# Optimization experiments

Hardware: AMD Instinct MI355X
Metric: run time of the kernel (lower is better)

The kernel has to match this reference:

```python
import jax, jax.numpy as jnp
import numpy as np


def _gcn(x, src, dst, W, b, n):
    # symmetric normalization: deg computed on edges WITH self-loops (weights 1)
    deg = jax.ops.segment_sum(jnp.ones_like(src, dtype=x.dtype), dst, num_segments=n)
    dinv = jnp.where(deg > 0, jax.lax.rsqrt(deg), 0.0)
    norm = dinv[src] * dinv[dst]              # [E+n]
    xw = x @ W                                # [n, out] transform first (cheaper)
    msg = xw[src] * norm[:, None]             # gather + edge scale
    return jax.ops.segment_sum(msg, dst, num_segments=n) + b


def setup_inputs() -> dict:
    key = jax.random.key(0)
    ks = jax.random.split(key, 8)
    N, E = 100_000, 1_280_000
    x = jax.random.normal(ks[0], (N, 18), dtype=jnp.float32)
    edge_index = jax.random.randint(ks[1], (2, E), 0, N, dtype=jnp.int32)
    W1 = jax.random.normal(ks[2], (18, 32), dtype=jnp.float32) * 0.2
    b1 = jnp.zeros((32,), dtype=jnp.float32)
    W2 = jax.random.normal(ks[3], (32, 64), dtype=jnp.float32) * 0.15
    b2 = jnp.zeros((64,), dtype=jnp.float32)
    Wfc = jax.random.normal(ks[4], (64, 2), dtype=jnp.float32) * 0.1
    bfc = jnp.zeros((2,), dtype=jnp.float32)
    return {"x": x, "edge_index": edge_index, "W1": W1, "b1": b1,
            "W2": W2, "b2": b2, "Wfc": Wfc, "bfc": bfc}


def reference(x, edge_index, W1, b1, W2, b2, Wfc, bfc):
    n = x.shape[0]
    loop = jnp.arange(n, dtype=edge_index.dtype)
    src = jnp.concatenate([edge_index[0], loop])   # add self-loops (PyG default)
    dst = jnp.concatenate([edge_index[1], loop])
    h = jax.nn.relu(_gcn(x, src, dst, W1, b1, n))
    h = jax.nn.relu(_gcn(h, src, dst, W2, b2, n))
    logits = h @ Wfc + bfc
    return jax.nn.log_softmax(logits, axis=1)
```

## Files before the change

### kernel.cpp

```cpp
#include <hip/hip_runtime.h>
#include <hip/hip_fp16.h>
#include <math.h>


#define TPB 256
#define BSH 8
#define BNODES 256
#define MAXBUCK 512
#define CH 8192
#define CAPSH 13
#define CAP (1 << CAPSH)

__global__ void k_part(const int* __restrict__ src, const int* __restrict__ dst,
                       int* __restrict__ bcursor, int* __restrict__ eb,
                       __half* __restrict__ u1h, __half* __restrict__ u2h,
                       int E, int n, int nbuck) {
    __shared__ int lh[MAXBUCK];
    __shared__ int lbase[MAXBUCK];
    int t = threadIdx.x;
    if (blockIdx.x == 0 && t < 32) {
        u1h[(size_t)n * 32 + t] = __float2half_rn(0.f);
        u2h[(size_t)n * 32 + t] = __float2half_rn(0.f);
    }
    int chunk0 = blockIdx.x * CH;
    int end = min(chunk0 + CH, E);
    const int4* dst4 = (const int4*)dst;
    const int4* src4 = (const int4*)src;
    for (int i = t; i < nbuck; i += TPB) lh[i] = 0;
    __syncthreads();
    for (int e4 = chunk0 / 4 + t; e4 * 4 < end; e4 += TPB) {
        int base = e4 * 4;
        int4 d = dst4[e4];
        if (base + 0 < end) atomicAdd(&lh[d.x >> BSH], 1);
        if (base + 1 < end) atomicAdd(&lh[d.y >> BSH], 1);
        if (base + 2 < end) atomicAdd(&lh[d.z >> BSH], 1);
        if (base + 3 < end) atomicAdd(&lh[d.w >> BSH], 1);
    }
    __syncthreads();
    for (int i = t; i < nbuck; i += TPB) {
        int c = lh[i];
        lbase[i] = c ? atomicAdd(&bcursor[i], c) : 0;
        lh[i] = 0;
    }
    __syncthreads();
    for (int e4 = chunk0 / 4 + t; e4 * 4 < end; e4 += TPB) {
        int base = e4 * 4;
        int4 d = dst4[e4];
        int4 s = src4[e4];
        #define PUT(c, sv) if (base + c < end) { \
            int b = (d.sv) >> BSH; \
            int r = lbase[b] + atomicAdd(&lh[b], 1); \
            if (r < CAP) \
                eb[((size_t)b << CAPSH) + r] = ((s.sv) << BSH) | ((d.sv) & (BNODES - 1)); }
        PUT(0, x) PUT(1, y) PUT(2, z) PUT(3, w)
        #undef PUT
    }
}

__global__ void k_bucket(const int* __restrict__ eb, const int* __restrict__ bcursor,
                         const float* __restrict__ x,
                         int* __restrict__ csr, int* __restrict__ row_start,
                         int* __restrict__ cnt4, float* __restrict__ dinv,
                         __half* __restrict__ u1h, int n) {
    __shared__ int lcnt[BNODES];
    __shared__ int lscan[BNODES];
    __shared__ float ldinv[BNODES];
    int b = blockIdx.x;
    int t = threadIdx.x;
    int node0 = b << BSH;
    int beg = b << CAPSH;
    int end = beg + min(bcursor[b], CAP);
    lcnt[t] = 0;
    __syncthreads();
    for (int i = beg + t; i < end; i += TPB)
        atomicAdd(&lcnt[eb[i] & (BNODES - 1)], 1);
    __syncthreads();
    int v = lcnt[t];
    int pad = (v + 3) & ~3;
    lscan[t] = pad;
    __syncthreads();
    for (int off = 1; off < TPB; off <<= 1) {
        int xx = (t >= off) ? lscan[t - off] : 0;
        __syncthreads();
        lscan[t] += xx;
        __syncthreads();
    }
    int pexcl = lscan[t] - pad;
    int node = node0 + t;
    float dv = rsqrtf(1.0f + (float)v);
    ldinv[t] = dv;
    if (node < n) {
        row_start[node] = beg + pexcl;
        cnt4[node] = pad >> 2;
        dinv[node] = dv;
    }
    __syncthreads();
    lcnt[t] = pexcl;
    __syncthreads();
    for (int i = beg + t; i < end; i += TPB) {
        int e = eb[i];
        int p = atomicAdd(&lcnt[e & (BNODES - 1)], 1);
        csr[beg + p] = e >> BSH;
    }
    __syncthreads();
    for (int p = v; p < pad; ++p) csr[beg + pexcl + p] = n;
    int nn = min(BNODES, n - node0);
    int tot = nn * 32;
    const float* xb = x + (size_t)node0 * 18;
    __half* ub = u1h + (size_t)node0 * 32;
    for (int i = t; i < tot; i += TPB) {
        int nl = i >> 5, f = i & 31;
        float val = (f < 18) ? xb[nl * 18 + f] * ldinv[nl] : 0.f;
        ub[i] = __float2half_rn(val);
    }
}

__global__ void k_fused1(const uint2* __restrict__ u1q, const int* __restrict__ row_start,
                         const int* __restrict__ cnt4, const int* __restrict__ csr,
                         const float* __restrict__ dinv, const float* __restrict__ W1,
                         const float* __restrict__ b1, __half* __restrict__ u2h,
                         int n) {
    __shared__ float lagg[4][8][33];
    int t = threadIdx.x;
    int lane = t & 63, wv = t >> 6;
    int q = lane & 7, grp = lane >> 3;
    int f = lane & 31, h = lane >> 5;
    float w1r[18];
#pragma unroll
    for (int k = 0; k < 18; ++k) w1r[k] = W1[k * 32 + f];
    float b1v = b1[f];
    int node0 = (blockIdx.x * 4 + wv) * 8;
    int node = node0 + grp;
    float a0 = 0.f, a1 = 0.f, a2 = 0.f, a3 = 0.f;
    if (node < n) {
        uint2 sv = u1q[(size_t)node * 8 + q];
        __half2* sh = (__half2*)&sv;
        float2 s01 = __half22float2(sh[0]), s23 = __half22float2(sh[1]);
        a0 = s01.x; a1 = s01.y; a2 = s23.x; a3 = s23.y;
        int beg = row_start[node];
        int it = cnt4[node];
        const int4* ip = (const int4*)(csr + beg);
        for (int i = 0; i < it; ++i) {
            int4 s = ip[i];
            uint2 v0 = u1q[(size_t)s.x * 8 + q];
            uint2 v1 = u1q[(size_t)s.y * 8 + q];
            uint2 v2 = u1q[(size_t)s.z * 8 + q];
            uint2 v3 = u1q[(size_t)s.w * 8 + q];
            __half2* p0 = (__half2*)&v0; __half2* p1 = (__half2*)&v1;
            __half2* p2 = (__half2*)&v2; __half2* p3 = (__half2*)&v3;
            float2 f00 = __half22float2(p0[0]), f01 = __half22float2(p0[1]);
            float2 f10 = __half22float2(p1[0]), f11 = __half22float2(p1[1]);
            float2 f20 = __half22float2(p2[0]), f21 = __half22float2(p2[1]);
            float2 f30 = __half22float2(p3[0]), f31 = __half22float2(p3[1]);
            a0 += (f00.x + f10.x) + (f20.x + f30.x);
            a1 += (f00.y + f10.y) + (f20.y + f30.y);
            a2 += (f01.x + f11.x) + (f21.x + f31.x);
            a3 += (f01.y + f11.y) + (f21.y + f31.y);
        }
    }
    lagg[wv][grp][4 * q + 0] = a0;
    lagg[wv][grp][4 * q + 1] = a1;
    lagg[wv][grp][4 * q + 2] = a2;
    lagg[wv][grp][4 * q + 3] = a3;
#pragma unroll
    for (int r = 0; r < 4; ++r) {
        int nl = 2 * r + h;
        int nodeT = node0 + nl;
        if (nodeT < n) {
            const float* rp = lagg[wv][nl];
            float a = 0.f;
#pragma unroll
            for (int k = 0; k < 18; ++k) a = fmaf(rp[k], w1r[k], a);
            float di = dinv[nodeT];
            u2h[(size_t)nodeT * 32 + f] =
                __float2half_rn(fmaxf(fmaf(di, a, b1v), 0.f) * di);
        }
    }
}

__global__ void k_fused2(const uint2* __restrict__ u2q, const int* __restrict__ row_start,
                         const int* __restrict__ cnt4, const int* __restrict__ csr,
                         const float* __restrict__ dinv, const float* __restrict__ W2,
                         const float* __restrict__ b2, const float* __restrict__ Wfc,
                         const float* __restrict__ bfc, float* __restrict__ out,
                         int n) {
    __shared__ float lagg[4][8][33];
    int t = threadIdx.x;
    int lane = t & 63, wv = t >> 6;
    int q = lane & 7, grp = lane >> 3;
    float w2r[32];
#pragma unroll
    for (int k = 0; k < 32; ++k) w2r[k] = W2[k * 64 + lane];
    float b2v = b2[lane];
    float wf0 = Wfc[lane * 2 + 0], wf1 = Wfc[lane * 2 + 1];
    float bf0 = bfc[0], bf1 = bfc[1];
    int node0 = (blockIdx.x * 4 + wv) * 8;
    int node = node0 + grp;
    float a0 = 0.f, a1 = 0.f, a2 = 0.f, a3 = 0.f;
    if (node < n) {
        uint2 sv = u2q[(size_t)node * 8 + q];
        __half2* sh = (__half2*)&sv;
        float2 s01 = __half22float2(sh[0]), s23 = __half22float2(sh[1]);
        a0 = s01.x; a1 = s01.y; a2 = s23.x; a3 = s23.y;
        int beg = row_start[node];
        int it = cnt4[node];
        const int4* ip = (const int4*)(csr + beg);
        for (int i = 0; i < it; ++i) {
            int4 s = ip[i];
            uint2 v0 = u2q[(size_t)s.x * 8 + q];
            uint2 v1 = u2q[(size_t)s.y * 8 + q];
            uint2 v2 = u2q[(size_t)s.z * 8 + q];
            uint2 v3 = u2q[(size_t)s.w * 8 + q];
            __half2* p0 = (__half2*)&v0; __half2* p1 = (__half2*)&v1;
            __half2* p2 = (__half2*)&v2; __half2* p3 = (__half2*)&v3;
            float2 f00 = __half22float2(p0[0]), f01 = __half22float2(p0[1]);
            float2 f10 = __half22float2(p1[0]), f11 = __half22float2(p1[1]);
            float2 f20 = __half22float2(p2[0]), f21 = __half22float2(p2[1]);
            float2 f30 = __half22float2(p3[0]), f31 = __half22float2(p3[1]);
            a0 += (f00.x + f10.x) + (f20.x + f30.x);
            a1 += (f00.y + f10.y) + (f20.y + f30.y);
            a2 += (f01.x + f11.x) + (f21.x + f31.x);
            a3 += (f01.y + f11.y) + (f21.y + f31.y);
        }
    }
    lagg[wv][grp][4 * q + 0] = a0;
    lagg[wv][grp][4 * q + 1] = a1;
    lagg[wv][grp][4 * q + 2] = a2;
    lagg[wv][grp][4 * q + 3] = a3;
#pragma unroll
    for (int r = 0; r < 8; ++r) {
        int nodeT = node0 + r;
        const float* rp = lagg[wv][r];
        float c0 = 0.f, c1 = 0.f, c2 = 0.f, c3 = 0.f;
#pragma unroll
        for (int k = 0; k < 32; k += 4) {
            c0 = fmaf(rp[k],     w2r[k],     c0);
            c1 = fmaf(rp[k + 1], w2r[k + 1], c1);
            c2 = fmaf(rp[k + 2], w2r[k + 2], c2);
            c3 = fmaf(rp[k + 3], w2r[k + 3], c3);
        }
        float a = (c0 + c1) + (c2 + c3);
        float v = (nodeT < n) ? fmaxf(fmaf(dinv[nodeT], a, b2v), 0.f) : 0.f;
        float l0 = v * wf0;
        float l1 = v * wf1;
#pragma unroll
        for (int off = 32; off >= 1; off >>= 1) {
            l0 += __shfl_xor(l0, off, 64);
            l1 += __shfl_xor(l1, off, 64);
        }
        if (lane == 0 && nodeT < n) {
            l0 += bf0;
            l1 += bf1;
            float m2 = fmaxf(l0, l1);
            float lse = m2 + logf(expf(l0 - m2) + expf(l1 - m2));
            out[nodeT * 2 + 0] = l0 - lse;
            out[nodeT * 2 + 1] = l1 - lse;
        }
    }
}

extern "C" void kernel_launch(void* const* d_in, const int* in_sizes, int n_in,
                              void* d_out, int out_size, void* d_ws, size_t ws_size,
                              hipStream_t stream) {
    const float* x   = (const float*)d_in[0];
    const int*   ei  = (const int*)d_in[1];
    const float* W1  = (const float*)d_in[2];
    const float* b1  = (const float*)d_in[3];
    const float* W2  = (const float*)d_in[4];
    const float* b2  = (const float*)d_in[5];
    const float* Wfc = (const float*)d_in[6];
    const float* bfc = (const float*)d_in[7];
    float* out = (float*)d_out;

    const int n = in_sizes[0] / 18;
    const int E = in_sizes[1] / 2;
    const int* src = ei;
    const int* dst = ei + E;
    const int nbuck = (n + BNODES - 1) >> BSH;

    char* w = (char*)d_ws;
    int*    bcursor   = (int*)w;     w += (size_t)nbuck * 4;
    int*    row_start = (int*)w;     w += (size_t)n * 4;
    int*    cnt4      = (int*)w;     w += (size_t)n * 4;
    float*  dinv      = (float*)w;   w += (size_t)n * 4;
    int*    eb        = (int*)w;     w += (size_t)nbuck * CAP * 4;
    int*    csr       = (int*)w;     w += (size_t)nbuck * CAP * 4;
    w = (char*)(((size_t)w + 63) & ~(size_t)63);
    __half* u1h       = (__half*)w;  w += (size_t)(n + 1) * 32 * 2;
    w = (char*)(((size_t)w + 63) & ~(size_t)63);
    __half* u2h       = (__half*)w;  w += (size_t)(n + 1) * 32 * 2;

    hipMemsetAsync(bcursor, 0, (size_t)nbuck * 4, stream);
    k_part<<<(E + CH - 1) / CH, TPB, 0, stream>>>(src, dst, bcursor, eb, u1h, u2h, E, n, nbuck);
    k_bucket<<<nbuck, TPB, 0, stream>>>(eb, bcursor, x, csr, row_start, cnt4, dinv, u1h, n);

    const int waves = (n + 7) / 8;
    const int blocksF = (waves + 3) / 4;

    k_fused1<<<blocksF, TPB, 0, stream>>>((const uint2*)u1h, row_start, cnt4, csr,
                                          dinv, W1, b1, u2h, n);
    k_fused2<<<blocksF, TPB, 0, stream>>>((const uint2*)u2h, row_start, cnt4, csr,
                                          dinv, W2, b2, Wfc, bfc, out, n);
}
```

Measured before the change: 180.4 us.

## Apply W1 before aggregation, degree-sort nodes per bucket, prefetch CSR indices

Layer 1's linear transform moves into the bucket kernel, so the first aggregation gathers 32-wide pre-transformed half features and k_fused1 only adds bias, ReLU and scaling. Each bucket bitonic-sorts its nodes by in-degree into a permutation, which the aggregation kernels use to group similar-degree nodes within a wave and reduce load imbalance. The CSR index load is software-prefetched one step ahead, which needs extra padding after csr. In exchange the bucket kernel gains a shared-memory sort and extra FMAs, the fused kernels add an indirection through perm, and perm writes can run past n for the last bucket, which the allocation sizes to cover.

After: 189.0 us. 1.05x slower.

```diff
diff --git a/kernel.cpp b/kernel.cpp
--- a/kernel.cpp
+++ b/kernel.cpp
@@ -58,13 +58,16 @@
 }
 
 __global__ void k_bucket(const int* __restrict__ eb, const int* __restrict__ bcursor,
-                         const float* __restrict__ x,
+                         const float* __restrict__ x, const float* __restrict__ W1,
                          int* __restrict__ csr, int* __restrict__ row_start,
                          int* __restrict__ cnt4, float* __restrict__ dinv,
+                         int* __restrict__ perm,
                          __half* __restrict__ u1h, int n) {
     __shared__ int lcnt[BNODES];
     __shared__ int lscan[BNODES];
     __shared__ float ldinv[BNODES];
+    __shared__ int lkey[BNODES];
+    __shared__ float xs[BNODES * 18];
     int b = blockIdx.x;
     int t = threadIdx.x;
     int node0 = b << BSH;
@@ -78,6 +81,7 @@
     int v = lcnt[t];
     int pad = (v + 3) & ~3;
     lscan[t] = pad;
+    lkey[t] = (v << 8) | t;
     __syncthreads();
     for (int off = 1; off < TPB; off <<= 1) {
         int xx = (t >= off) ? lscan[t - off] : 0;
@@ -104,44 +108,61 @@
     }
     __syncthreads();
     for (int p = v; p < pad; ++p) csr[beg + pexcl + p] = n;
+    for (int k = 2; k <= BNODES; k <<= 1) {
+        for (int j = k >> 1; j > 0; j >>= 1) {
+            int ixj = t ^ j;
+            int mine = lkey[t], other = lkey[ixj];
+            bool up = ((t & k) == 0);
+            int mn = min(mine, other), mx = max(mine, other);
+            int keep = ((ixj > t) == up) ? mn : mx;
+            __syncthreads();
+            lkey[t] = keep;
+            __syncthreads();
+        }
+    }
+    perm[node0 + t] = node0 + (lkey[t] & (BNODES - 1));
     int nn = min(BNODES, n - node0);
-    int tot = nn * 32;
     const float* xb = x + (size_t)node0 * 18;
+    int tot18 = nn * 18;
+    for (int i = t; i < tot18; i += TPB) xs[i] = xb[i];
+    __syncthreads();
+    int f = t & 31, g = t >> 5;
+    float w1r[18];
+#pragma unroll
+    for (int k = 0; k < 18; ++k) w1r[k] = W1[k * 32 + f];
     __half* ub = u1h + (size_t)node0 * 32;
-    for (int i = t; i < tot; i += TPB) {
-        int nl = i >> 5, f = i & 31;
-        float val = (f < 18) ? xb[nl * 18 + f] * ldinv[nl] : 0.f;
-        ub[i] = __float2half_rn(val);
+    for (int nl = g; nl < nn; nl += 8) {
+        const float* rp = &xs[nl * 18];
+        float a = 0.f;
+#pragma unroll
+        for (int k = 0; k < 18; ++k) a = fmaf(rp[k], w1r[k], a);
+        ub[nl * 32 + f] = __float2half_rn(a * ldinv[nl]);
     }
 }
 
 __global__ void k_fused1(const uint2* __restrict__ u1q, const int* __restrict__ row_start,
                          const int* __restrict__ cnt4, const int* __restrict__ csr,
-                         const float* __restrict__ dinv, const float* __restrict__ W1,
+                         const float* __restrict__ dinv, const int* __restrict__ perm,
                          const float* __restrict__ b1, __half* __restrict__ u2h,
                          int n) {
-    __shared__ float lagg[4][8][33];
     int t = threadIdx.x;
     int lane = t & 63, wv = t >> 6;
     int q = lane & 7, grp = lane >> 3;
-    int f = lane & 31, h = lane >> 5;
-    float w1r[18];
-#pragma unroll
-    for (int k = 0; k < 18; ++k) w1r[k] = W1[k * 32 + f];
-    float b1v = b1[f];
-    int node0 = (blockIdx.x * 4 + wv) * 8;
-    int node = node0 + grp;
-    float a0 = 0.f, a1 = 0.f, a2 = 0.f, a3 = 0.f;
-    if (node < n) {
-        uint2 sv = u1q[(size_t)node * 8 + q];
-        __half2* sh = (__half2*)&sv;
-        float2 s01 = __half22float2(sh[0]), s23 = __half22float2(sh[1]);
-        a0 = s01.x; a1 = s01.y; a2 = s23.x; a3 = s23.y;
-        int beg = row_start[node];
-        int it = cnt4[node];
-        const int4* ip = (const int4*)(csr + beg);
+    int slot = (blockIdx.x * 4 + wv) * 8 + grp;
+    int node = perm[slot];
+    if (node >= n) return;
+    float4 bb = ((const float4*)b1)[q];
+    uint2 sv = u1q[(size_t)node * 8 + q];
+    __half2* sh = (__half2*)&sv;
+    float2 s01 = __half22float2(sh[0]), s23 = __half22float2(sh[1]);
+    float a0 = s01.x, a1 = s01.y, a2 = s23.x, a3 = s23.y;
+    int beg = row_start[node];
+    int it = cnt4[node];
+    const int4* ip = (const int4*)(csr + beg);
+    if (it > 0) {
+        int4 s = ip[0];
         for (int i = 0; i < it; ++i) {
-            int4 s = ip[i];
+            int4 nx = ip[i + 1];
             uint2 v0 = u1q[(size_t)s.x * 8 + q];
             uint2 v1 = u1q[(size_t)s.y * 8 + q];
             uint2 v2 = u1q[(size_t)s.z * 8 + q];
@@ -156,31 +177,25 @@
             a1 += (f00.y + f10.y) + (f20.y + f30.y);
             a2 += (f01.x + f11.x) + (f21.x + f31.x);
             a3 += (f01.y + f11.y) + (f21.y + f31.y);
-        }
-    }
-    lagg[wv][grp][4 * q + 0] = a0;
-    lagg[wv][grp][4 * q + 1] = a1;
-    lagg[wv][grp][4 * q + 2] = a2;
-    lagg[wv][grp][4 * q + 3] = a3;
-#pragma unroll
-    for (int r = 0; r < 4; ++r) {
-        int nl = 2 * r + h;
-        int nodeT = node0 + nl;
-        if (nodeT < n) {
-            const float* rp = lagg[wv][nl];
-            float a = 0.f;
-#pragma unroll
-            for (int k = 0; k < 18; ++k) a = fmaf(rp[k], w1r[k], a);
-            float di = dinv[nodeT];
-            u2h[(size_t)nodeT * 32 + f] =
-                __float2half_rn(fmaxf(fmaf(di, a, b1v), 0.f) * di);
-        }
-    }
+            s = nx;
+        }
+    }
+    float di = dinv[node];
+    float r0 = fmaxf(fmaf(di, a0, bb.x), 0.f) * di;
+    float r1 = fmaxf(fmaf(di, a1, bb.y), 0.f) * di;
+    float r2 = fmaxf(fmaf(di, a2, bb.z), 0.f) * di;
+    float r3 = fmaxf(fmaf(di, a3, bb.w), 0.f) * di;
+    uint2 st;
+    __half2* sp = (__half2*)&st;
+    sp[0].x = __float2half_rn(r0); sp[0].y = __float2half_rn(r1);
+    sp[1].x = __float2half_rn(r2); sp[1].y = __float2half_rn(r3);
+    ((uint2*)u2h)[(size_t)node * 8 + q] = st;
 }
 
 __global__ void k_fused2(const uint2* __restrict__ u2q, const int* __restrict__ row_start,
                          const int* __restrict__ cnt4, const int* __restrict__ csr,
-                         const float* __restrict__ dinv, const float* __restrict__ W2,
+                         const float* __restrict__ dinv, const int* __restrict__ perm,
+                         const float* __restrict__ W2,
                          const float* __restrict__ b2, const float* __restrict__ Wfc,
                          const float* __restrict__ bfc, float* __restrict__ out,
                          int n) {
@@ -194,8 +209,8 @@
     float b2v = b2[lane];
     float wf0 = Wfc[lane * 2 + 0], wf1 = Wfc[lane * 2 + 1];
     float bf0 = bfc[0], bf1 = bfc[1];
-    int node0 = (blockIdx.x * 4 + wv) * 8;
-    int node = node0 + grp;
+    int slot0 = (blockIdx.x * 4 + wv) * 8;
+    int node = perm[slot0 + grp];
     float a0 = 0.f, a1 = 0.f, a2 = 0.f, a3 = 0.f;
     if (node < n) {
         uint2 sv = u2q[(size_t)node * 8 + q];
@@ -205,22 +220,26 @@
         int beg = row_start[node];
         int it = cnt4[node];
         const int4* ip = (const int4*)(csr + beg);
-        for (int i = 0; i < it; ++i) {
-            int4 s = ip[i];
-            uint2 v0 = u2q[(size_t)s.x * 8 + q];
-            uint2 v1 = u2q[(size_t)s.y * 8 + q];
-            uint2 v2 = u2q[(size_t)s.z * 8 + q];
-            uint2 v3 = u2q[(size_t)s.w * 8 + q];
-            __half2* p0 = (__half2*)&v0; __half2* p1 = (__half2*)&v1;
-            __half2* p2 = (__half2*)&v2; __half2* p3 = (__half2*)&v3;
-            float2 f00 = __half22float2(p0[0]), f01 = __half22float2(p0[1]);
-            float2 f10 = __half22float2(p1[0]), f11 = __half22float2(p1[1]);
-            float2 f20 = __half22float2(p2[0]), f21 = __half22float2(p2[1]);
-            float2 f30 = __half22float2(p3[0]), f31 = __half22float2(p3[1]);
-            a0 += (f00.x + f10.x) + (f20.x + f30.x);
-            a1 += (f00.y + f10.y) + (f20.y + f30.y);
-            a2 += (f01.x + f11.x) + (f21.x + f31.x);
-            a3 += (f01.y + f11.y) + (f21.y + f31.y);
+        if (it > 0) {
+            int4 s = ip[0];
+            for (int i = 0; i < it; ++i) {
+                int4 nx = ip[i + 1];
+                uint2 v0 = u2q[(size_t)s.x * 8 + q];
+                uint2 v1 = u2q[(size_t)s.y * 8 + q];
+                uint2 v2 = u2q[(size_t)s.z * 8 + q];
+                uint2 v3 = u2q[(size_t)s.w * 8 + q];
+                __half2* p0 = (__half2*)&v0; __half2* p1 = (__half2*)&v1;
+                __half2* p2 = (__half2*)&v2; __half2* p3 = (__half2*)&v3;
+                float2 f00 = __half22float2(p0[0]), f01 = __half22float2(p0[1]);
+                float2 f10 = __half22float2(p1[0]), f11 = __half22float2(p1[1]);
+                float2 f20 = __half22float2(p2[0]), f21 = __half22float2(p2[1]);
+                float2 f30 = __half22float2(p3[0]), f31 = __half22float2(p3[1]);
+                a0 += (f00.x + f10.x) + (f20.x + f30.x);
+                a1 += (f00.y + f10.y) + (f20.y + f30.y);
+                a2 += (f01.x + f11.x) + (f21.x + f31.x);
+                a3 += (f01.y + f11.y) + (f21.y + f31.y);
+                s = nx;
+            }
         }
     }
     lagg[wv][grp][4 * q + 0] = a0;
@@ -229,7 +248,7 @@
     lagg[wv][grp][4 * q + 3] = a3;
 #pragma unroll
     for (int r = 0; r < 8; ++r) {
-        int nodeT = node0 + r;
+        int nodeT = perm[slot0 + r];
         const float* rp = lagg[wv][r];
         float c0 = 0.f, c1 = 0.f, c2 = 0.f, c3 = 0.f;
 #pragma unroll
@@ -283,8 +302,9 @@
     int*    row_start = (int*)w;     w += (size_t)n * 4;
     int*    cnt4      = (int*)w;     w += (size_t)n * 4;
     float*  dinv      = (float*)w;   w += (size_t)n * 4;
+    int*    perm      = (int*)w;     w += (size_t)nbuck * BNODES * 4;
     int*    eb        = (int*)w;     w += (size_t)nbuck * CAP * 4;
-    int*    csr       = (int*)w;     w += (size_t)nbuck * CAP * 4;
+    int*    csr       = (int*)w;     w += (size_t)nbuck * CAP * 4 + 64;
     w = (char*)(((size_t)w + 63) & ~(size_t)63);
     __half* u1h       = (__half*)w;  w += (size_t)(n + 1) * 32 * 2;
     w = (char*)(((size_t)w + 63) & ~(size_t)63);
@@ -292,13 +312,13 @@
 
     hipMemsetAsync(bcursor, 0, (size_t)nbuck * 4, stream);
     k_part<<<(E + CH - 1) / CH, TPB, 0, stream>>>(src, dst, bcursor, eb, u1h, u2h, E, n, nbuck);
-    k_bucket<<<nbuck, TPB, 0, stream>>>(eb, bcursor, x, csr, row_start, cnt4, dinv, u1h, n);
-
-    const int waves = (n + 7) / 8;
-    const int blocksF = (waves + 3) / 4;
+    k_bucket<<<nbuck, TPB, 0, stream>>>(eb, bcursor, x, W1, csr, row_start, cnt4,
+                                        dinv, perm, u1h, n);
+
+    const int blocksF = nbuck * 8;
 
     k_fused1<<<blocksF, TPB, 0, stream>>>((const uint2*)u1h, row_start, cnt4, csr,
-                                          dinv, W1, b1, u2h, n);
+                                          dinv, perm, b1, u2h, n);
     k_fused2<<<blocksF, TPB, 0, stream>>>((const uint2*)u2h, row_start, cnt4, csr,
-                                          dinv, W2, b2, Wfc, bfc, out, n);
-}
+                                          dinv, perm, W2, b2, Wfc, bfc, out, n);
+}
```
